# Kernel tuning notes

Measured on AMD Instinct MI355X. Metric: run time of the kernel, lower is better.

## Reference

```python
import jax, jax.numpy as jnp
import numpy as np

STATE_DIM = 256
LATENT_DIM = 64
HIDDEN = 64
NUM_EMB = 2048
BATCH = 32768


def setup_inputs() -> dict:
    key = jax.random.key(0)
    ks = jax.random.split(key, 10)
    s = lambda *sh: 1.0 / np.sqrt(sh[0])
    return {
        "x": jax.random.normal(ks[0], (BATCH, STATE_DIM), dtype=jnp.float32),
        # encoder: Linear(state_dim, 64) -> ReLU -> Linear(64, latent_dim)
        "enc_w1": jax.random.uniform(ks[1], (STATE_DIM, HIDDEN), jnp.float32, -s(STATE_DIM), s(STATE_DIM)),
        "enc_b1": jax.random.uniform(ks[2], (HIDDEN,), jnp.float32, -s(STATE_DIM), s(STATE_DIM)),
        "enc_w2": jax.random.uniform(ks[3], (HIDDEN, LATENT_DIM), jnp.float32, -s(HIDDEN), s(HIDDEN)),
        "enc_b2": jax.random.uniform(ks[4], (LATENT_DIM,), jnp.float32, -s(HIDDEN), s(HIDDEN)),
        # codebook
        "emb": jax.random.normal(ks[5], (NUM_EMB, LATENT_DIM), dtype=jnp.float32),
        # decoder: Linear(latent_dim, 64) -> ReLU -> Linear(64, state_dim)
        "dec_w1": jax.random.uniform(ks[6], (LATENT_DIM, HIDDEN), jnp.float32, -s(LATENT_DIM), s(LATENT_DIM)),
        "dec_b1": jax.random.uniform(ks[7], (HIDDEN,), jnp.float32, -s(LATENT_DIM), s(LATENT_DIM)),
        "dec_w2": jax.random.uniform(ks[8], (HIDDEN, STATE_DIM), jnp.float32, -s(HIDDEN), s(HIDDEN)),
        "dec_b2": jax.random.uniform(ks[9], (STATE_DIM,), jnp.float32, -s(HIDDEN), s(HIDDEN)),
    }


def reference(x, enc_w1, enc_b1, enc_w2, enc_b2, emb, dec_w1, dec_b1, dec_w2, dec_b2):
    # encoder MLP: z_e [B, latent]
    h = jax.nn.relu(x @ enc_w1 + enc_b1)
    z_e = h @ enc_w2 + enc_b2
    # squared euclidean distances to codebook, expanded form: [B, K]
    # ||z - e||^2 = ||z||^2 - 2 z.e + ||e||^2  (same argmin as broadcast form)
    d = (jnp.sum(z_e * z_e, axis=1, keepdims=True)
         - 2.0 * (z_e @ emb.T)
         + jnp.sum(emb * emb, axis=1)[None, :])
    z_q_idx = jnp.argmin(d, axis=1)           # [B]
    z_q = emb[z_q_idx]                        # [B, latent]
    # decoder MLP
    hd = jax.nn.relu(z_q @ dec_w1 + dec_b1)
    x_recon = hd @ dec_w2 + dec_b2
    return (x_recon, z_e, z_q)
```

## Files before the change

### kernel.cpp

```cpp
#include <hip/hip_runtime.h>

#define BATCH   32768
#define SD      256
#define LD      64
#define HDIM    64
#define NEMB    2048
#define REFINE_THR_Q 5e-4f

typedef short  short8 __attribute__((ext_vector_type(8)));
typedef float  f32x4  __attribute__((ext_vector_type(4)));

__device__ __forceinline__ unsigned short f2bf(float f) {
    unsigned int u = __float_as_uint(f);
    u = (u + 0x7FFFu + ((u >> 16) & 1u)) >> 16;
    return (unsigned short)u;
}
__device__ __forceinline__ float bf2f(unsigned short h) {
    return __uint_as_float(((unsigned int)h) << 16);
}

__global__ __launch_bounds__(256) void k0_prep(const float* __restrict__ emb,
                                               float* __restrict__ e2q,
                                               unsigned short* __restrict__ eh,
                                               unsigned short* __restrict__ el,
                                               int* __restrict__ count) {
    int k = blockIdx.x * 256 + threadIdx.x;
    if (k == 0) *count = 0;
    const float* er = emb + (size_t)k * LD;
    unsigned short hrow[LD], lrow[LD];
    float s = 0.f;
#pragma unroll
    for (int q = 0; q < LD; ++q) {
        float v = er[q];
        s += v * v;
        unsigned short h = f2bf(v);
        hrow[q] = h;
        lrow[q] = f2bf(v - bf2f(h));
    }
    e2q[k] = -0.5f * s;
    short8* dh = (short8*)(eh + (size_t)k * LD);
    short8* dl = (short8*)(el + (size_t)k * LD);
#pragma unroll
    for (int q = 0; q < 8; ++q) {
        dh[q] = *(short8*)&hrow[q * 8];
        dl[q] = *(short8*)&lrow[q * 8];
    }
}

__global__ __launch_bounds__(512, 4) void k_enc(const float* __restrict__ x,
                                                const float* __restrict__ w1,
                                                const float* __restrict__ b1,
                                                const float* __restrict__ w2,
                                                const float* __restrict__ b2,
                                                float* __restrict__ zOut,
                                                unsigned short* __restrict__ zh,
                                                unsigned short* __restrict__ zl) {
    __shared__ float smem[20480];
    float* w1s = smem;
    float* xs  = smem + 16384;
    int tid = threadIdx.x;
    {
        const float4* src = (const float4*)w1;
        float4* dst = (float4*)w1s;
#pragma unroll
        for (int t = 0; t < 8; ++t) dst[tid + 512 * t] = src[tid + 512 * t];
    }
    int r0 = blockIdx.x * 64;
    int sr = tid >> 3;
    int sq = tid & 7;
    const float* xrow = x + (size_t)(r0 + sr) * SD + sq * 4;
    *(float4*)&xs[sr * 32 + sq * 4] = *(const float4*)xrow;
    __syncthreads();

    int lane = tid & 63;
    int w = tid >> 6;
    float acc[8];
#pragma unroll
    for (int r = 0; r < 8; ++r) acc[r] = 0.f;

    for (int c = 0; c < 8; ++c) {
        float4 nv;
        if (c < 7) nv = *(const float4*)(xrow + (c + 1) * 32);
        const float* xb = &xs[(c & 1) * 2048 + (w * 8) * 32];
        int kb = c * 32;
#pragma unroll
        for (int i0 = 0; i0 < 32; i0 += 8) {
            float wf[8];
#pragma unroll
            for (int jj = 0; jj < 8; ++jj) wf[jj] = w1s[(kb + i0 + jj) * HDIM + lane];
#pragma unroll
            for (int r = 0; r < 8; ++r) {
                const float* xr = xb + r * 32 + i0;
                float4 xa = *(const float4*)xr;
                float4 xc = *(const float4*)(xr + 4);
                acc[r] += xa.x * wf[0] + xa.y * wf[1] + xa.z * wf[2] + xa.w * wf[3]
                        + xc.x * wf[4] + xc.y * wf[5] + xc.z * wf[6] + xc.w * wf[7];
            }
        }
        __syncthreads();
        if (c < 7) *(float4*)&xs[((c + 1) & 1) * 2048 + sr * 32 + sq * 4] = nv;
        __syncthreads();
    }

    float* hs  = smem;
    float* w2s = smem + 4096;
    float bb1 = b1[lane];
#pragma unroll
    for (int r = 0; r < 8; ++r)
        hs[(w * 8 + r) * 64 + lane] = fmaxf(acc[r] + bb1, 0.f);
    {
        const float4* src = (const float4*)w2;
        float4* dst = (float4*)w2s;
        dst[tid] = src[tid];
        dst[tid + 512] = src[tid + 512];
    }
    __syncthreads();

    const float* hb = &hs[(w * 8) * 64];
    float ac2[8];
#pragma unroll
    for (int r = 0; r < 8; ++r) ac2[r] = 0.f;

    for (int j0 = 0; j0 < HDIM; j0 += 8) {
        float wf[8];
#pragma unroll
        for (int jj = 0; jj < 8; ++jj) wf[jj] = w2s[(j0 + jj) * LD + lane];
#pragma unroll
        for (int r = 0; r < 8; ++r) {
            const float* hr = hb + r * 64 + j0;
            float4 ha = *(const float4*)hr;
            float4 hc = *(const float4*)(hr + 4);
            ac2[r] += ha.x * wf[0] + ha.y * wf[1] + ha.z * wf[2] + ha.w * wf[3]
                    + hc.x * wf[4] + hc.y * wf[5] + hc.z * wf[6] + hc.w * wf[7];
        }
    }
    float bb2 = b2[lane];
#pragma unroll
    for (int r = 0; r < 8; ++r) {
        float z = ac2[r] + bb2;
        size_t o = (size_t)(r0 + w * 8 + r) * LD + lane;
        zOut[o] = z;
        unsigned short h = f2bf(z);
        zh[o] = h;
        zl[o] = f2bf(z - bf2f(h));
    }
}

#define K2_LOAD(P, t) do {                                                  \
    const unsigned short* ph_ = ehp + (size_t)(t) * 16 * LD;                \
    const unsigned short* pl_ = elp + (size_t)(t) * 16 * LD;                \
    P##a0 = *(const short8*)(ph_);                                          \
    P##a1 = *(const short8*)(ph_ + 32);                                     \
    P##a2 = *(const short8*)(pl_);                                          \
    P##a3 = *(const short8*)(pl_ + 32);                                     \
    P##e2 = *(const f32x4*)(e2q + cbase + (t) * 16 + hi * 4);               \
} while (0)

#define K2_COMP(P, t) do {                                                  \
    f32x4 acc_[4];                                                          \
    _Pragma("unroll")                                                       \
    for (int g = 0; g < 4; ++g) {                                           \
        f32x4 c_;                                                           \
        c_ = __builtin_amdgcn_mfma_f32_16x16x32_bf16(P##a0, bh[g][0], P##e2, 0, 0, 0); \
        c_ = __builtin_amdgcn_mfma_f32_16x16x32_bf16(P##a1, bh[g][1], c_, 0, 0, 0);    \
        c_ = __builtin_amdgcn_mfma_f32_16x16x32_bf16(P##a2, bh[g][0], c_, 0, 0, 0);    \
        c_ = __builtin_amdgcn_mfma_f32_16x16x32_bf16(P##a3, bh[g][1], c_, 0, 0, 0);    \
        c_ = __builtin_amdgcn_mfma_f32_16x16x32_bf16(P##a0, bl[g][0], c_, 0, 0, 0);    \
        c_ = __builtin_amdgcn_mfma_f32_16x16x32_bf16(P##a1, bl[g][1], c_, 0, 0, 0);    \
        acc_[g] = c_;                                                       \
    }                                                                       \
    _Pragma("unroll")                                                       \
    for (int g = 0; g < 4; ++g) {                                           \
        float m_ = fmaxf(fmaxf(acc_[g][0], acc_[g][1]),                     \
                         fmaxf(acc_[g][2], acc_[g][3]));                    \
        bool win_ = (m_ > bb[g]);                                           \
        qv[g] = win_ ? acc_[g] : qv[g];                                     \
        tt[g] = win_ ? (t) : tt[g];                                         \
        b2v[g] = fmaxf(b2v[g], fminf(bb[g], m_));                           \
        bb[g] = fmaxf(bb[g], m_);                                           \
    }                                                                       \
} while (0)

__global__ __launch_bounds__(256, 2) void k2_mfma(const unsigned short* __restrict__ zh,
                                                  const unsigned short* __restrict__ zl,
                                                  const unsigned short* __restrict__ eh,
                                                  const unsigned short* __restrict__ el,
                                                  const float* __restrict__ e2q,
                                                  int* __restrict__ idx,
                                                  int* __restrict__ list,
                                                  int* __restrict__ count) {
    int tid  = threadIdx.x;
    int lane = tid & 63;
    int w    = tid >> 6;
    int rb   = blockIdx.x * 64;
    int lo   = lane & 15;
    int hi   = lane >> 4;

    short8 bh[4][2], bl[4][2];
#pragma unroll
    for (int g = 0; g < 4; ++g) {
        size_t zo = (size_t)(rb + g * 16 + lo) * LD + hi * 8;
        bh[g][0] = *(const short8*)(zh + zo);
        bh[g][1] = *(const short8*)(zh + zo + 32);
        bl[g][0] = *(const short8*)(zl + zo);
        bl[g][1] = *(const short8*)(zl + zo + 32);
    }

    float bb[4], b2v[4];
    f32x4 qv[4];
    int   tt[4];
#pragma unroll
    for (int g = 0; g < 4; ++g) {
        bb[g] = -3.0e38f; b2v[g] = -3.0e38f; tt[g] = 0;
        qv[g][0] = qv[g][1] = qv[g][2] = qv[g][3] = -3.0e38f;
    }

    const int cbase = w * (NEMB / 4);
    const unsigned short* ehp = eh + (size_t)(cbase + lo) * LD + hi * 8;
    const unsigned short* elp = el + (size_t)(cbase + lo) * LD + hi * 8;

    short8 Aa0, Aa1, Aa2, Aa3; f32x4 Ae2;
    short8 Ba0, Ba1, Ba2, Ba3; f32x4 Be2;
    short8 Ca0, Ca1, Ca2, Ca3; f32x4 Ce2;

    K2_LOAD(A, 0);
    K2_LOAD(B, 1);
    K2_LOAD(C, 2);

    for (int tb = 0; tb < 27; tb += 3) {
        K2_COMP(A, tb);     K2_LOAD(A, tb + 3);
        K2_COMP(B, tb + 1); K2_LOAD(B, tb + 4);
        K2_COMP(C, tb + 2); K2_LOAD(C, tb + 5);
    }
    K2_COMP(A, 27); K2_LOAD(A, 30);
    K2_COMP(B, 28); K2_LOAD(B, 31);
    K2_COMP(C, 29);
    K2_COMP(A, 30);
    K2_COMP(B, 31);

    float ss[4];
    int   ii[4];
#pragma unroll
    for (int g = 0; g < 4; ++g) {
        float s0 = qv[g][0], s1 = qv[g][1], s2 = qv[g][2], s3 = qv[g][3];
        float M01 = fmaxf(s0, s1), L01 = fminf(s0, s1);
        float M23 = fmaxf(s2, s3), L23 = fminf(s2, s3);
        int   d01 = (s1 > s0) ? 1 : 0;
        int   d23 = (s3 > s2) ? 3 : 2;
        bool  cp  = (M23 > M01);
        float within2 = fmaxf(fminf(M01, M23), cp ? L23 : L01);
        int   dd  = cp ? d23 : d01;
        ii[g] = cbase + tt[g] * 16 + hi * 4 + dd;
        ss[g] = fmaxf(b2v[g], within2);
    }

#pragma unroll
    for (int off = 16; off <= 32; off <<= 1) {
#pragma unroll
        for (int g = 0; g < 4; ++g) {
            float ob = __shfl_xor(bb[g], off);
            float os = __shfl_xor(ss[g], off);
            int   oi = __shfl_xor(ii[g], off);
            ss[g] = fmaxf(fmaxf(fminf(bb[g], ob), os), ss[g]);
            ii[g] = (ob > bb[g]) ? oi : ii[g];
            bb[g] = fmaxf(bb[g], ob);
        }
    }

    __shared__ float Lb[4][64];
    __shared__ float Ls[4][64];
    __shared__ int   Li[4][64];
    if (lane < 16) {
#pragma unroll
        for (int g = 0; g < 4; ++g) {
            Lb[w][g * 16 + lane] = bb[g];
            Ls[w][g * 16 + lane] = ss[g];
            Li[w][g * 16 + lane] = ii[g];
        }
    }
    __syncthreads();

    if (tid < 64) {
        float B = Lb[0][tid], S = Ls[0][tid];
        int   I = Li[0][tid];
#pragma unroll
        for (int w2 = 1; w2 < 4; ++w2) {
            float ob = Lb[w2][tid], os = Ls[w2][tid];
            int   oi = Li[w2][tid];
            S = fmaxf(fmaxf(fminf(B, ob), os), S);
            I = (ob > B) ? oi : I;
            B = fmaxf(B, ob);
        }
        idx[rb + tid] = I;
        if (B - S < REFINE_THR_Q) {
            int p = atomicAdd(count, 1);
            list[p] = rb + tid;
        }
    }
}

__global__ __launch_bounds__(256) void k3_refine(const float* __restrict__ z,
                                                 const float* __restrict__ emb,
                                                 const int* __restrict__ count,
                                                 const int* __restrict__ list,
                                                 int* __restrict__ idx) {
    __shared__ double sv[256];
    __shared__ int    sx[256];
    int tid = threadIdx.x;
    int n = *count;
    for (int g = blockIdx.x; g < n; g += gridDim.x) {
        int row = list[g];
        const float4* zr4 = (const float4*)(z + (size_t)row * LD);
        float4 zv[16];
#pragma unroll
        for (int q = 0; q < 16; ++q) zv[q] = zr4[q];

        double best = 1.0e300;
        int bi = NEMB;
#pragma unroll 2
        for (int c = 0; c < 8; ++c) {
            int k = tid * 8 + c;
            const float4* er = (const float4*)(emb + (size_t)k * LD);
            double d0 = 0.0, d1 = 0.0, d2 = 0.0, d3 = 0.0;
#pragma unroll
            for (int q = 0; q < 16; ++q) {
                float4 e4 = er[q];
                double tx = (double)zv[q].x - (double)e4.x;
                double ty = (double)zv[q].y - (double)e4.y;
                double tz = (double)zv[q].z - (double)e4.z;
                double tw = (double)zv[q].w - (double)e4.w;
                d0 += tx * tx; d1 += ty * ty; d2 += tz * tz; d3 += tw * tw;
            }
            double d = (d0 + d1) + (d2 + d3);
            if (d < best) { best = d; bi = k; }
        }
        sv[tid] = best; sx[tid] = bi;
        __syncthreads();
        for (int s = 128; s > 0; s >>= 1) {
            if (tid < s) {
                if (sv[tid + s] < sv[tid] ||
                    (sv[tid + s] == sv[tid] && sx[tid + s] < sx[tid])) {
                    sv[tid] = sv[tid + s]; sx[tid] = sx[tid + s];
                }
            }
            __syncthreads();
        }
        if (tid == 0) idx[row] = sx[0];
        __syncthreads();
    }
}

__global__ __launch_bounds__(512, 4) void k_dec(const int* __restrict__ idx,
                                                const float* __restrict__ emb,
                                                const float* __restrict__ w1,
                                                const float* __restrict__ b1,
                                                const float* __restrict__ w2,
                                                const float* __restrict__ b2,
                                                float* __restrict__ xrec,
                                                float* __restrict__ zq) {
    __shared__ float smem[12288];
    float* w1s = smem;
    float* zqs = smem + 4096;
    float* hds = smem + 8192;
    int tid = threadIdx.x;
    int r0 = blockIdx.x * 64;
    {
        const float4* src = (const float4*)w1;
        float4* dst = (float4*)w1s;
        dst[tid] = src[tid];
        dst[tid + 512] = src[tid + 512];
    }
    {
        float4* dst = (float4*)zqs;
#pragma unroll
        for (int t = 0; t < 2; ++t) {
            int f = tid + 512 * t;
            int r = f >> 4, q = f & 15;
            int ix = idx[r0 + r];
            dst[f] = *(const float4*)(emb + (size_t)ix * LD + q * 4);
        }
    }
    __syncthreads();
    {
        const float4* s = (const float4*)zqs;
        float4* d = (float4*)(zq + (size_t)r0 * LD);
        d[tid] = s[tid];
        d[tid + 512] = s[tid + 512];
    }

    int lane = tid & 63;
    int w = tid >> 6;
    const float* zb = &zqs[(w * 8) * 64];

    float acc[8];
#pragma unroll
    for (int r = 0; r < 8; ++r) acc[r] = 0.f;

    for (int j0 = 0; j0 < LD; j0 += 8) {
        float wf[8];
#pragma unroll
        for (int jj = 0; jj < 8; ++jj) wf[jj] = w1s[(j0 + jj) * HDIM + lane];
#pragma unroll
        for (int r = 0; r < 8; ++r) {
            const float* zr = zb + r * 64 + j0;
            float4 za = *(const float4*)zr;
            float4 zc = *(const float4*)(zr + 4);
            acc[r] += za.x * wf[0] + za.y * wf[1] + za.z * wf[2] + za.w * wf[3]
                    + zc.x * wf[4] + zc.y * wf[5] + zc.z * wf[6] + zc.w * wf[7];
        }
    }
    float bb1 = b1[lane];
#pragma unroll
    for (int r = 0; r < 8; ++r)
        hds[(w * 8 + r) * 64 + lane] = fmaxf(acc[r] + bb1, 0.f);
    __syncthreads();

    float* w2s = smem;
    for (int ct = 0; ct < 4; ++ct) {
#pragma unroll
        for (int t = 0; t < 2; ++t) {
            int f = tid + 512 * t;
            int j = f >> 4, q = f & 15;
            *(float4*)&w2s[j * 64 + q * 4] =
                *(const float4*)(w2 + (size_t)j * SD + ct * 64 + q * 4);
        }
        __syncthreads();

        float a2[8];
#pragma unroll
        for (int r = 0; r < 8; ++r) a2[r] = 0.f;
        const float* hb = &hds[(w * 8) * 64];
        for (int j0 = 0; j0 < HDIM; j0 += 8) {
            float wf[8];
#pragma unroll
            for (int jj = 0; jj < 8; ++jj) wf[jj] = w2s[(j0 + jj) * 64 + lane];
#pragma unroll
            for (int r = 0; r < 8; ++r) {
                const float* hr = hb + r * 64 + j0;
                float4 ha = *(const float4*)hr;
                float4 hc = *(const float4*)(hr + 4);
                a2[r] += ha.x * wf[0] + ha.y * wf[1] + ha.z * wf[2] + ha.w * wf[3]
                       + hc.x * wf[4] + hc.y * wf[5] + hc.z * wf[6] + hc.w * wf[7];
            }
        }
        float bbo = b2[ct * 64 + lane];
#pragma unroll
        for (int r = 0; r < 8; ++r)
            xrec[(size_t)(r0 + w * 8 + r) * SD + ct * 64 + lane] = a2[r] + bbo;
        __syncthreads();
    }
}

extern "C" void kernel_launch(void* const* d_in, const int* in_sizes, int n_in,
                              void* d_out, int out_size, void* d_ws, size_t ws_size,
                              hipStream_t stream) {
    const float* x   = (const float*)d_in[0];
    const float* ew1 = (const float*)d_in[1];
    const float* eb1 = (const float*)d_in[2];
    const float* ew2 = (const float*)d_in[3];
    const float* eb2 = (const float*)d_in[4];
    const float* emb = (const float*)d_in[5];
    const float* dw1 = (const float*)d_in[6];
    const float* db1 = (const float*)d_in[7];
    const float* dw2 = (const float*)d_in[8];
    const float* db2 = (const float*)d_in[9];

    float* out  = (float*)d_out;
    float* xrec = out;
    float* zE   = out + (size_t)BATCH * SD;
    float* zQ   = zE + (size_t)BATCH * LD;

    char* xb = (char*)xrec;
    unsigned short* zh  = (unsigned short*)xb;
    unsigned short* zl  = (unsigned short*)(xb + (4u << 20));
    unsigned short* eh  = (unsigned short*)(xb + (8u << 20));
    unsigned short* el  = (unsigned short*)(xb + (8u << 20) + (NEMB * LD * 2));
    float*          e2q = (float*)(xb + (9u << 20));

    char* ws = (char*)d_ws;
    int*  count = (int*)ws;
    int*  idxA  = (int*)(ws + 16384);
    int*  list  = (int*)(ws + 16384 + (size_t)BATCH * 4);

    hipLaunchKernelGGL(k0_prep,   dim3(NEMB / 256), dim3(256), 0, stream, emb, e2q, eh, el, count);
    hipLaunchKernelGGL(k_enc,     dim3(BATCH / 64), dim3(512), 0, stream, x, ew1, eb1, ew2, eb2, zE, zh, zl);
    hipLaunchKernelGGL(k2_mfma,   dim3(BATCH / 64), dim3(256), 0, stream, zh, zl, eh, el, e2q, idxA, list, count);
    hipLaunchKernelGGL(k3_refine, dim3(128),        dim3(256), 0, stream, zE, emb, count, list, idxA);
    hipLaunchKernelGGL(k_dec,     dim3(BATCH / 64), dim3(512), 0, stream, idxA, emb, dw1, db1, dw2, db2, xrec, zQ);
}
```

Baseline: 135.5 us.

## Restructure encoder/decoder MLPs to row-per-lane with split-K across waves

The encoder and decoder kernels are rewritten so each lane owns one batch row and keeps 64 accumulators in registers. Weights are read directly from global memory with wave-uniform addresses, so they become scalar or broadcast loads, and the K dimension is split across four waves with an LDS reduction. This drops the shared-memory weight staging and the per-row LDS broadcasts of the old tiling. In exchange it raises register pressure (64-float accumulator arrays), adds reduction passes through LDS, and reads x with a per-lane row stride that is uncoalesced.

```diff
diff --git a/kernel.cpp b/kernel.cpp
--- a/kernel.cpp
+++ b/kernel.cpp
@@ -47,7 +47,7 @@
     }
 }
 
-__global__ __launch_bounds__(512, 4) void k_enc(const float* __restrict__ x,
+__global__ __launch_bounds__(256, 2) void k_enc(const float* __restrict__ x,
                                                 const float* __restrict__ w1,
                                                 const float* __restrict__ b1,
                                                 const float* __restrict__ w2,
@@ -55,94 +55,88 @@
                                                 float* __restrict__ zOut,
                                                 unsigned short* __restrict__ zh,
                                                 unsigned short* __restrict__ zl) {
-    __shared__ float smem[20480];
-    float* w1s = smem;
-    float* xs  = smem + 16384;
-    int tid = threadIdx.x;
-    {
-        const float4* src = (const float4*)w1;
-        float4* dst = (float4*)w1s;
-#pragma unroll
-        for (int t = 0; t < 8; ++t) dst[tid + 512 * t] = src[tid + 512 * t];
-    }
-    int r0 = blockIdx.x * 64;
-    int sr = tid >> 3;
-    int sq = tid & 7;
-    const float* xrow = x + (size_t)(r0 + sr) * SD + sq * 4;
-    *(float4*)&xs[sr * 32 + sq * 4] = *(const float4*)xrow;
-    __syncthreads();
-
+    __shared__ float red[2][64][66];
+    __shared__ float hs[64 * 65];
+    int tid  = threadIdx.x;
     int lane = tid & 63;
-    int w = tid >> 6;
-    float acc[8];
-#pragma unroll
-    for (int r = 0; r < 8; ++r) acc[r] = 0.f;
-
-    for (int c = 0; c < 8; ++c) {
-        float4 nv;
-        if (c < 7) nv = *(const float4*)(xrow + (c + 1) * 32);
-        const float* xb = &xs[(c & 1) * 2048 + (w * 8) * 32];
-        int kb = c * 32;
-#pragma unroll
-        for (int i0 = 0; i0 < 32; i0 += 8) {
-            float wf[8];
-#pragma unroll
-            for (int jj = 0; jj < 8; ++jj) wf[jj] = w1s[(kb + i0 + jj) * HDIM + lane];
-#pragma unroll
-            for (int r = 0; r < 8; ++r) {
-                const float* xr = xb + r * 32 + i0;
-                float4 xa = *(const float4*)xr;
-                float4 xc = *(const float4*)(xr + 4);
-                acc[r] += xa.x * wf[0] + xa.y * wf[1] + xa.z * wf[2] + xa.w * wf[3]
-                        + xc.x * wf[4] + xc.y * wf[5] + xc.z * wf[6] + xc.w * wf[7];
+    int w    = __builtin_amdgcn_readfirstlane(tid >> 6);
+    int r0   = blockIdx.x * 64;
+    int row  = r0 + lane;
+
+    float acc[64];
+#pragma unroll
+    for (int j = 0; j < 64; ++j) acc[j] = 0.f;
+    {
+        const float* xrow = x + (size_t)row * SD + w * 64;
+        const float* wbase = w1 + (size_t)w * 64 * HDIM;
+        for (int k4 = 0; k4 < 16; ++k4) {
+            float4 xk = *(const float4*)(xrow + k4 * 4);
+            const float* wr = wbase + (size_t)k4 * 4 * HDIM;
+#pragma unroll
+            for (int j = 0; j < 64; ++j) {
+                acc[j] = fmaf(xk.x, wr[j],            acc[j]);
+                acc[j] = fmaf(xk.y, wr[HDIM + j],     acc[j]);
+                acc[j] = fmaf(xk.z, wr[2 * HDIM + j], acc[j]);
+                acc[j] = fmaf(xk.w, wr[3 * HDIM + j], acc[j]);
             }
         }
-        __syncthreads();
-        if (c < 7) *(float4*)&xs[((c + 1) & 1) * 2048 + sr * 32 + sq * 4] = nv;
-        __syncthreads();
-    }
-
-    float* hs  = smem;
-    float* w2s = smem + 4096;
-    float bb1 = b1[lane];
-#pragma unroll
-    for (int r = 0; r < 8; ++r)
-        hs[(w * 8 + r) * 64 + lane] = fmaxf(acc[r] + bb1, 0.f);
-    {
-        const float4* src = (const float4*)w2;
-        float4* dst = (float4*)w2s;
-        dst[tid] = src[tid];
-        dst[tid + 512] = src[tid + 512];
-    }
-    __syncthreads();
-
-    const float* hb = &hs[(w * 8) * 64];
-    float ac2[8];
-#pragma unroll
-    for (int r = 0; r < 8; ++r) ac2[r] = 0.f;
-
-    for (int j0 = 0; j0 < HDIM; j0 += 8) {
-        float wf[8];
-#pragma unroll
-        for (int jj = 0; jj < 8; ++jj) wf[jj] = w2s[(j0 + jj) * LD + lane];
-#pragma unroll
-        for (int r = 0; r < 8; ++r) {
-            const float* hr = hb + r * 64 + j0;
-            float4 ha = *(const float4*)hr;
-            float4 hc = *(const float4*)(hr + 4);
-            ac2[r] += ha.x * wf[0] + ha.y * wf[1] + ha.z * wf[2] + ha.w * wf[3]
-                    + hc.x * wf[4] + hc.y * wf[5] + hc.z * wf[6] + hc.w * wf[7];
-        }
-    }
-    float bb2 = b2[lane];
-#pragma unroll
-    for (int r = 0; r < 8; ++r) {
-        float z = ac2[r] + bb2;
-        size_t o = (size_t)(r0 + w * 8 + r) * LD + lane;
-        zOut[o] = z;
-        unsigned short h = f2bf(z);
-        zh[o] = h;
-        zl[o] = f2bf(z - bf2f(h));
+    }
+    if (w >= 2) {
+#pragma unroll
+        for (int j = 0; j < 64; ++j) red[w - 2][j][lane] = acc[j];
+    }
+    __syncthreads();
+    if (w < 2) {
+#pragma unroll
+        for (int j = 0; j < 64; ++j) red[w][j][lane] += acc[j];
+    }
+    __syncthreads();
+    {
+        int i = tid & 63, jg = tid >> 6;
+#pragma unroll
+        for (int jj = 0; jj < 16; ++jj) {
+            int j = jg * 16 + jj;
+            float hv = red[0][j][i] + red[1][j][i] + b1[j];
+            hs[i * 65 + j] = fmaxf(hv, 0.f);
+        }
+    }
+    __syncthreads();
+
+    float ac2[64];
+#pragma unroll
+    for (int j = 0; j < 64; ++j) ac2[j] = 0.f;
+    {
+        const float* wbase = w2 + (size_t)w * 16 * LD;
+        for (int k2 = 0; k2 < 16; ++k2) {
+            float hk = hs[lane * 65 + w * 16 + k2];
+            const float* wr = wbase + (size_t)k2 * LD;
+#pragma unroll
+            for (int j = 0; j < 64; ++j) ac2[j] = fmaf(hk, wr[j], ac2[j]);
+        }
+    }
+    if (w >= 2) {
+#pragma unroll
+        for (int j = 0; j < 64; ++j) red[w - 2][j][lane] = ac2[j];
+    }
+    __syncthreads();
+    if (w < 2) {
+#pragma unroll
+        for (int j = 0; j < 64; ++j) red[w][j][lane] += ac2[j];
+    }
+    __syncthreads();
+    {
+        int j = tid & 63, ig = tid >> 6;
+        float bj = b2[j];
+#pragma unroll
+        for (int ii = 0; ii < 16; ++ii) {
+            int i = ig * 16 + ii;
+            float z = red[0][j][i] + red[1][j][i] + bj;
+            size_t o = (size_t)(r0 + i) * LD + j;
+            zOut[o] = z;
+            unsigned short hb = f2bf(z);
+            zh[o] = hb;
+            zl[o] = f2bf(z - bf2f(hb));
+        }
     }
 }
 
@@ -350,7 +344,7 @@
     }
 }
 
-__global__ __launch_bounds__(512, 4) void k_dec(const int* __restrict__ idx,
+__global__ __launch_bounds__(256, 2) void k_dec(const int* __restrict__ idx,
                                                 const float* __restrict__ emb,
                                                 const float* __restrict__ w1,
                                                 const float* __restrict__ b1,
@@ -358,96 +352,78 @@
                                                 const float* __restrict__ b2,
                                                 float* __restrict__ xrec,
                                                 float* __restrict__ zq) {
-    __shared__ float smem[12288];
-    float* w1s = smem;
-    float* zqs = smem + 4096;
-    float* hds = smem + 8192;
-    int tid = threadIdx.x;
-    int r0 = blockIdx.x * 64;
-    {
-        const float4* src = (const float4*)w1;
-        float4* dst = (float4*)w1s;
-        dst[tid] = src[tid];
-        dst[tid + 512] = src[tid + 512];
-    }
-    {
-        float4* dst = (float4*)zqs;
-#pragma unroll
-        for (int t = 0; t < 2; ++t) {
-            int f = tid + 512 * t;
-            int r = f >> 4, q = f & 15;
-            int ix = idx[r0 + r];
-            dst[f] = *(const float4*)(emb + (size_t)ix * LD + q * 4);
-        }
-    }
-    __syncthreads();
-    {
-        const float4* s = (const float4*)zqs;
-        float4* d = (float4*)(zq + (size_t)r0 * LD);
-        d[tid] = s[tid];
-        d[tid + 512] = s[tid + 512];
-    }
-
+    __shared__ float red[2][64][66];
+    __shared__ float hds[64 * 65];
+    int tid  = threadIdx.x;
     int lane = tid & 63;
-    int w = tid >> 6;
-    const float* zb = &zqs[(w * 8) * 64];
-
-    float acc[8];
-#pragma unroll
-    for (int r = 0; r < 8; ++r) acc[r] = 0.f;
-
-    for (int j0 = 0; j0 < LD; j0 += 8) {
-        float wf[8];
-#pragma unroll
-        for (int jj = 0; jj < 8; ++jj) wf[jj] = w1s[(j0 + jj) * HDIM + lane];
-#pragma unroll
-        for (int r = 0; r < 8; ++r) {
-            const float* zr = zb + r * 64 + j0;
-            float4 za = *(const float4*)zr;
-            float4 zc = *(const float4*)(zr + 4);
-            acc[r] += za.x * wf[0] + za.y * wf[1] + za.z * wf[2] + za.w * wf[3]
-                    + zc.x * wf[4] + zc.y * wf[5] + zc.z * wf[6] + zc.w * wf[7];
-        }
-    }
-    float bb1 = b1[lane];
-#pragma unroll
-    for (int r = 0; r < 8; ++r)
-        hds[(w * 8 + r) * 64 + lane] = fmaxf(acc[r] + bb1, 0.f);
-    __syncthreads();
-
-    float* w2s = smem;
-    for (int ct = 0; ct < 4; ++ct) {
-#pragma unroll
-        for (int t = 0; t < 2; ++t) {
-            int f = tid + 512 * t;
-            int j = f >> 4, q = f & 15;
-            *(float4*)&w2s[j * 64 + q * 4] =
-                *(const float4*)(w2 + (size_t)j * SD + ct * 64 + q * 4);
-        }
-        __syncthreads();
-
-        float a2[8];
-#pragma unroll
-        for (int r = 0; r < 8; ++r) a2[r] = 0.f;
-        const float* hb = &hds[(w * 8) * 64];
-        for (int j0 = 0; j0 < HDIM; j0 += 8) {
-            float wf[8];
-#pragma unroll
-            for (int jj = 0; jj < 8; ++jj) wf[jj] = w2s[(j0 + jj) * 64 + lane];
-#pragma unroll
-            for (int r = 0; r < 8; ++r) {
-                const float* hr = hb + r * 64 + j0;
-                float4 ha = *(const float4*)hr;
-                float4 hc = *(const float4*)(hr + 4);
-                a2[r] += ha.x * wf[0] + ha.y * wf[1] + ha.z * wf[2] + ha.w * wf[3]
-                       + hc.x * wf[4] + hc.y * wf[5] + hc.z * wf[6] + hc.w * wf[7];
+    int w    = __builtin_amdgcn_readfirstlane(tid >> 6);
+    int r0   = blockIdx.x * 64;
+    int row  = r0 + lane;
+    int ix   = idx[row];
+
+    float accA[64];
+#pragma unroll
+    for (int j = 0; j < 64; ++j) accA[j] = 0.f;
+    {
+        const float* er  = emb + (size_t)ix * LD + w * 16;
+        float* zqr = zq + (size_t)row * LD + w * 16;
+        const float* wbase = w1 + (size_t)w * 16 * HDIM;
+#pragma unroll
+        for (int k4 = 0; k4 < 4; ++k4) {
+            float4 zk = *(const float4*)(er + k4 * 4);
+            *(float4*)(zqr + k4 * 4) = zk;
+            const float* wr = wbase + (size_t)k4 * 4 * HDIM;
+#pragma unroll
+            for (int j = 0; j < 64; ++j) {
+                accA[j] = fmaf(zk.x, wr[j],            accA[j]);
+                accA[j] = fmaf(zk.y, wr[HDIM + j],     accA[j]);
+                accA[j] = fmaf(zk.z, wr[2 * HDIM + j], accA[j]);
+                accA[j] = fmaf(zk.w, wr[3 * HDIM + j], accA[j]);
             }
         }
-        float bbo = b2[ct * 64 + lane];
-#pragma unroll
-        for (int r = 0; r < 8; ++r)
-            xrec[(size_t)(r0 + w * 8 + r) * SD + ct * 64 + lane] = a2[r] + bbo;
-        __syncthreads();
+    }
+    if (w >= 2) {
+#pragma unroll
+        for (int j = 0; j < 64; ++j) red[w - 2][j][lane] = accA[j];
+    }
+    __syncthreads();
+    if (w < 2) {
+#pragma unroll
+        for (int j = 0; j < 64; ++j) red[w][j][lane] += accA[j];
+    }
+    __syncthreads();
+    {
+        int i = tid & 63, jg = tid >> 6;
+#pragma unroll
+        for (int jj = 0; jj < 16; ++jj) {
+            int j = jg * 16 + jj;
+            float hv = red[0][j][i] + red[1][j][i] + b1[j];
+            hds[i * 65 + j] = fmaxf(hv, 0.f);
+        }
+    }
+    __syncthreads();
+
+    float accB[64];
+#pragma unroll
+    for (int j = 0; j < 64; ++j) accB[j] = 0.f;
+    for (int k = 0; k < 64; ++k) {
+        float hk = hds[lane * 65 + k];
+        const float* wr = w2 + (size_t)k * SD + w * 64;
+#pragma unroll
+        for (int j = 0; j < 64; ++j) accB[j] = fmaf(hk, wr[j], accB[j]);
+    }
+    {
+        float* xr = xrec + (size_t)row * SD + w * 64;
+        const float* bb = b2 + w * 64;
+#pragma unroll
+        for (int q = 0; q < 16; ++q) {
+            float4 v;
+            v.x = accB[q * 4 + 0] + bb[q * 4 + 0];
+            v.y = accB[q * 4 + 1] + bb[q * 4 + 1];
+            v.z = accB[q * 4 + 2] + bb[q * 4 + 2];
+            v.w = accB[q * 4 + 3] + bb[q * 4 + 3];
+            *(float4*)(xr + q * 4) = v;
+        }
     }
 }
 
@@ -483,8 +459,8 @@
     int*  list  = (int*)(ws + 16384 + (size_t)BATCH * 4);
 
     hipLaunchKernelGGL(k0_prep,   dim3(NEMB / 256), dim3(256), 0, stream, emb, e2q, eh, el, count);
-    hipLaunchKernelGGL(k_enc,     dim3(BATCH / 64), dim3(512), 0, stream, x, ew1, eb1, ew2, eb2, zE, zh, zl);
+    hipLaunchKernelGGL(k_enc,     dim3(BATCH / 64), dim3(256), 0, stream, x, ew1, eb1, ew2, eb2, zE, zh, zl);
     hipLaunchKernelGGL(k2_mfma,   dim3(BATCH / 64), dim3(256), 0, stream, zh, zl, eh, el, e2q, idxA, list, count);
     hipLaunchKernelGGL(k3_refine, dim3(128),        dim3(256), 0, stream, zE, emb, count, list, idxA);
-    hipLaunchKernelGGL(k_dec,     dim3(BATCH / 64), dim3(512), 0, stream, idxA, emb, dw1, db1, dw2, db2, xrec, zQ);
-}
+    hipLaunchKernelGGL(k_dec,     dim3(BATCH / 64), dim3(256), 0, stream, idxA, emb, dw1, db1, dw2, db2, xrec, zQ);
+}
```

Result: slower. 141.9 us (+4.7%).

## Move decoder MLP to bf16x3 split MFMA with pre-split transposed weights

Applied to the files above, without the earlier changes.

The decoder kernel swaps its scalar FP32 LDS-tiled matmuls for 16x16x32 bf16 MFMA instructions. Each operand is split into high and low bf16 parts and combined with three MFMAs to keep near-FP32 accuracy. A new prep kernel transposes and splits the decoder weights into workspace, and the kernel now reads weight fragments straight from global memory instead of staging them in LDS. This adds one small launch and extra MFMA work per tile, and the result can differ slightly from the FP32 reference.

```diff
diff --git a/kernel.cpp b/kernel.cpp
--- a/kernel.cpp
+++ b/kernel.cpp
@@ -44,6 +44,29 @@
     for (int q = 0; q < 8; ++q) {
         dh[q] = *(short8*)&hrow[q * 8];
         dl[q] = *(short8*)&lrow[q * 8];
+    }
+}
+
+__global__ __launch_bounds__(256) void k0b_wsplit(const float* __restrict__ w1,
+                                                  const float* __restrict__ w2,
+                                                  unsigned short* __restrict__ w1h,
+                                                  unsigned short* __restrict__ w1l,
+                                                  unsigned short* __restrict__ w2h,
+                                                  unsigned short* __restrict__ w2l) {
+    int b = blockIdx.x;
+    int t = threadIdx.x;
+    if (b < 16) {
+        int e = b * 256 + t;
+        int j = e >> 6, k = e & 63;
+        float v = w1[k * HDIM + j];
+        unsigned short h = f2bf(v);
+        w1h[e] = h; w1l[e] = f2bf(v - bf2f(h));
+    } else {
+        int e = (b - 16) * 256 + t;
+        int j = e >> 6, k = e & 63;
+        float v = w2[k * SD + j];
+        unsigned short h = f2bf(v);
+        w2h[e] = h; w2l[e] = f2bf(v - bf2f(h));
     }
 }
 
@@ -350,104 +373,98 @@
     }
 }
 
-__global__ __launch_bounds__(512, 4) void k_dec(const int* __restrict__ idx,
+__global__ __launch_bounds__(256, 2) void k_dec(const int* __restrict__ idx,
                                                 const float* __restrict__ emb,
-                                                const float* __restrict__ w1,
+                                                const unsigned short* __restrict__ w1h,
+                                                const unsigned short* __restrict__ w1l,
                                                 const float* __restrict__ b1,
-                                                const float* __restrict__ w2,
+                                                const unsigned short* __restrict__ w2h,
+                                                const unsigned short* __restrict__ w2l,
                                                 const float* __restrict__ b2,
                                                 float* __restrict__ xrec,
                                                 float* __restrict__ zq) {
-    __shared__ float smem[12288];
-    float* w1s = smem;
-    float* zqs = smem + 4096;
-    float* hds = smem + 8192;
-    int tid = threadIdx.x;
-    int r0 = blockIdx.x * 64;
+    __shared__ float hds[4][16 * 68];
+    int tid  = threadIdx.x;
+    int lane = tid & 63;
+    int w    = tid >> 6;
+    int lo   = lane & 15;
+    int hi   = lane >> 4;
+    int rb   = blockIdx.x * 64 + w * 16;
+    int row  = rb + lo;
+    int ix   = idx[row];
+
+    short8 zah[2], zal[2];
     {
-        const float4* src = (const float4*)w1;
-        float4* dst = (float4*)w1s;
-        dst[tid] = src[tid];
-        dst[tid + 512] = src[tid + 512];
-    }
-    {
-        float4* dst = (float4*)zqs;
-#pragma unroll
-        for (int t = 0; t < 2; ++t) {
-            int f = tid + 512 * t;
-            int r = f >> 4, q = f & 15;
-            int ix = idx[r0 + r];
-            dst[f] = *(const float4*)(emb + (size_t)ix * LD + q * 4);
-        }
+        const float* er  = emb + (size_t)ix * LD + hi * 8;
+        float* zqr = zq + (size_t)row * LD + hi * 8;
+#pragma unroll
+        for (int kt = 0; kt < 2; ++kt) {
+            float4 a = *(const float4*)(er + kt * 32);
+            float4 b = *(const float4*)(er + kt * 32 + 4);
+            *(float4*)(zqr + kt * 32) = a;
+            *(float4*)(zqr + kt * 32 + 4) = b;
+            float v[8] = {a.x, a.y, a.z, a.w, b.x, b.y, b.z, b.w};
+            unsigned short hh[8], ll[8];
+#pragma unroll
+            for (int q = 0; q < 8; ++q) {
+                unsigned short hb = f2bf(v[q]);
+                hh[q] = hb;
+                ll[q] = f2bf(v[q] - bf2f(hb));
+            }
+            zah[kt] = *(short8*)hh;
+            zal[kt] = *(short8*)ll;
+        }
+    }
+
+#pragma unroll
+    for (int jt = 0; jt < 4; ++jt) {
+        float bj = b1[jt * 16 + lo];
+        f32x4 c = {bj, bj, bj, bj};
+#pragma unroll
+        for (int kt = 0; kt < 2; ++kt) {
+            short8 bh8 = *(const short8*)(w1h + (jt * 16 + lo) * LD + kt * 32 + hi * 8);
+            short8 bl8 = *(const short8*)(w1l + (jt * 16 + lo) * LD + kt * 32 + hi * 8);
+            c = __builtin_amdgcn_mfma_f32_16x16x32_bf16(zah[kt], bh8, c, 0, 0, 0);
+            c = __builtin_amdgcn_mfma_f32_16x16x32_bf16(zah[kt], bl8, c, 0, 0, 0);
+            c = __builtin_amdgcn_mfma_f32_16x16x32_bf16(zal[kt], bh8, c, 0, 0, 0);
+        }
+#pragma unroll
+        for (int r = 0; r < 4; ++r)
+            hds[w][(hi * 4 + r) * 68 + jt * 16 + lo] = fmaxf(c[r], 0.f);
     }
     __syncthreads();
-    {
-        const float4* s = (const float4*)zqs;
-        float4* d = (float4*)(zq + (size_t)r0 * LD);
-        d[tid] = s[tid];
-        d[tid + 512] = s[tid + 512];
-    }
-
-    int lane = tid & 63;
-    int w = tid >> 6;
-    const float* zb = &zqs[(w * 8) * 64];
-
-    float acc[8];
-#pragma unroll
-    for (int r = 0; r < 8; ++r) acc[r] = 0.f;
-
-    for (int j0 = 0; j0 < LD; j0 += 8) {
-        float wf[8];
-#pragma unroll
-        for (int jj = 0; jj < 8; ++jj) wf[jj] = w1s[(j0 + jj) * HDIM + lane];
-#pragma unroll
-        for (int r = 0; r < 8; ++r) {
-            const float* zr = zb + r * 64 + j0;
-            float4 za = *(const float4*)zr;
-            float4 zc = *(const float4*)(zr + 4);
-            acc[r] += za.x * wf[0] + za.y * wf[1] + za.z * wf[2] + za.w * wf[3]
-                    + zc.x * wf[4] + zc.y * wf[5] + zc.z * wf[6] + zc.w * wf[7];
-        }
-    }
-    float bb1 = b1[lane];
-#pragma unroll
-    for (int r = 0; r < 8; ++r)
-        hds[(w * 8 + r) * 64 + lane] = fmaxf(acc[r] + bb1, 0.f);
-    __syncthreads();
-
-    float* w2s = smem;
-    for (int ct = 0; ct < 4; ++ct) {
-#pragma unroll
-        for (int t = 0; t < 2; ++t) {
-            int f = tid + 512 * t;
-            int j = f >> 4, q = f & 15;
-            *(float4*)&w2s[j * 64 + q * 4] =
-                *(const float4*)(w2 + (size_t)j * SD + ct * 64 + q * 4);
-        }
-        __syncthreads();
-
-        float a2[8];
-#pragma unroll
-        for (int r = 0; r < 8; ++r) a2[r] = 0.f;
-        const float* hb = &hds[(w * 8) * 64];
-        for (int j0 = 0; j0 < HDIM; j0 += 8) {
-            float wf[8];
-#pragma unroll
-            for (int jj = 0; jj < 8; ++jj) wf[jj] = w2s[(j0 + jj) * 64 + lane];
-#pragma unroll
-            for (int r = 0; r < 8; ++r) {
-                const float* hr = hb + r * 64 + j0;
-                float4 ha = *(const float4*)hr;
-                float4 hc = *(const float4*)(hr + 4);
-                a2[r] += ha.x * wf[0] + ha.y * wf[1] + ha.z * wf[2] + ha.w * wf[3]
-                       + hc.x * wf[4] + hc.y * wf[5] + hc.z * wf[6] + hc.w * wf[7];
-            }
-        }
-        float bbo = b2[ct * 64 + lane];
-#pragma unroll
-        for (int r = 0; r < 8; ++r)
-            xrec[(size_t)(r0 + w * 8 + r) * SD + ct * 64 + lane] = a2[r] + bbo;
-        __syncthreads();
+
+    short8 hah[2], hal[2];
+#pragma unroll
+    for (int kt = 0; kt < 2; ++kt) {
+        float4 a = *(const float4*)&hds[w][lo * 68 + kt * 32 + hi * 8];
+        float4 b = *(const float4*)&hds[w][lo * 68 + kt * 32 + hi * 8 + 4];
+        float v[8] = {a.x, a.y, a.z, a.w, b.x, b.y, b.z, b.w};
+        unsigned short hh[8], ll[8];
+#pragma unroll
+        for (int q = 0; q < 8; ++q) {
+            unsigned short hb = f2bf(v[q]);
+            hh[q] = hb;
+            ll[q] = f2bf(v[q] - bf2f(hb));
+        }
+        hah[kt] = *(short8*)hh;
+        hal[kt] = *(short8*)ll;
+    }
+
+    for (int jt = 0; jt < 16; ++jt) {
+        float bj = b2[jt * 16 + lo];
+        f32x4 c = {bj, bj, bj, bj};
+#pragma unroll
+        for (int kt = 0; kt < 2; ++kt) {
+            short8 bh8 = *(const short8*)(w2h + (jt * 16 + lo) * LD + kt * 32 + hi * 8);
+            short8 bl8 = *(const short8*)(w2l + (jt * 16 + lo) * LD + kt * 32 + hi * 8);
+            c = __builtin_amdgcn_mfma_f32_16x16x32_bf16(hah[kt], bh8, c, 0, 0, 0);
+            c = __builtin_amdgcn_mfma_f32_16x16x32_bf16(hah[kt], bl8, c, 0, 0, 0);
+            c = __builtin_amdgcn_mfma_f32_16x16x32_bf16(hal[kt], bh8, c, 0, 0, 0);
+        }
+#pragma unroll
+        for (int r = 0; r < 4; ++r)
+            xrec[(size_t)(rb + hi * 4 + r) * SD + jt * 16 + lo] = c[r];
     }
 }
 
@@ -480,11 +497,16 @@
     char* ws = (char*)d_ws;
     int*  count = (int*)ws;
     int*  idxA  = (int*)(ws + 16384);
-    int*  list  = (int*)(ws + 16384 + (size_t)BATCH * 4);
-
-    hipLaunchKernelGGL(k0_prep,   dim3(NEMB / 256), dim3(256), 0, stream, emb, e2q, eh, el, count);
-    hipLaunchKernelGGL(k_enc,     dim3(BATCH / 64), dim3(512), 0, stream, x, ew1, eb1, ew2, eb2, zE, zh, zl);
-    hipLaunchKernelGGL(k2_mfma,   dim3(BATCH / 64), dim3(256), 0, stream, zh, zl, eh, el, e2q, idxA, list, count);
-    hipLaunchKernelGGL(k3_refine, dim3(128),        dim3(256), 0, stream, zE, emb, count, list, idxA);
-    hipLaunchKernelGGL(k_dec,     dim3(BATCH / 64), dim3(512), 0, stream, idxA, emb, dw1, db1, dw2, db2, xrec, zQ);
-}
+    int*  list  = (int*)(ws + 147456);
+    unsigned short* w1h = (unsigned short*)(ws + 278528);
+    unsigned short* w1l = (unsigned short*)(ws + 286720);
+    unsigned short* w2h = (unsigned short*)(ws + 294912);
+    unsigned short* w2l = (unsigned short*)(ws + 327680);
+
+    hipLaunchKernelGGL(k0_prep,    dim3(NEMB / 256), dim3(256), 0, stream, emb, e2q, eh, el, count);
+    hipLaunchKernelGGL(k0b_wsplit, dim3(80),         dim3(256), 0, stream, dw1, dw2, w1h, w1l, w2h, w2l);
+    hipLaunchKernelGGL(k_enc,      dim3(BATCH / 64), dim3(512), 0, stream, x, ew1, eb1, ew2, eb2, zE, zh, zl);
+    hipLaunchKernelGGL(k2_mfma,    dim3(BATCH / 64), dim3(256), 0, stream, zh, zl, eh, el, e2q, idxA, list, count);
+    hipLaunchKernelGGL(k3_refine,  dim3(128),        dim3(256), 0, stream, zE, emb, count, list, idxA);
+    hipLaunchKernelGGL(k_dec,      dim3(BATCH / 64), dim3(256), 0, stream, idxA, emb, w1h, w1l, db1, w2h, w2l, db2, xrec, zQ);
+}
```

Result: faster. 129.9 us (-4.1%).
